# Optimization experiments

Measured on AMD Instinct MI355X. Metric: run time of the kernel, lower is better.

The kernel has to match this reference:

```python
import jax, jax.numpy as jnp
import numpy as np

D_MODEL = 1024
N_HEADS = 16
D_H = D_MODEL // N_HEADS
B, S = 2, 2048


def setup_inputs() -> dict:
    key = jax.random.key(0)
    ks = jax.random.split(key, 12)
    s = 1.0 / np.sqrt(D_MODEL)
    inp = {
        "Q": jax.random.normal(ks[0], (B, S, D_MODEL), jnp.float32),
        "K": jax.random.normal(ks[1], (B, S, D_MODEL), jnp.float32),
        "V": jax.random.normal(ks[2], (B, S, D_MODEL), jnp.float32),
        # causal mask: True means masked out (matches masked_fill semantics)
        "masked": jnp.broadcast_to(~jnp.tril(jnp.ones((S, S), bool)), (B, S, S)),
        "WQ_w": jax.random.uniform(ks[3], (D_MODEL, D_MODEL), jnp.float32, -s, s),
        "WQ_b": jax.random.uniform(ks[4], (D_MODEL,), jnp.float32, -s, s),
        "WK_w": jax.random.uniform(ks[5], (D_MODEL, D_MODEL), jnp.float32, -s, s),
        "WK_b": jax.random.uniform(ks[6], (D_MODEL,), jnp.float32, -s, s),
        "WV_w": jax.random.uniform(ks[7], (D_MODEL, D_MODEL), jnp.float32, -s, s),
        "WV_b": jax.random.uniform(ks[8], (D_MODEL,), jnp.float32, -s, s),
        "Wo_w": jax.random.uniform(ks[9], (D_MODEL, D_MODEL), jnp.float32, -s, s),
        "Wo_b": jax.random.uniform(ks[10], (D_MODEL,), jnp.float32, -s, s),
    }
    return inp


def reference(Q, K, V, masked, WQ_w, WQ_b, WK_w, WK_b, WV_w, WV_b, Wo_w, Wo_b):
    b = Q.shape[0]
    # torch Linear: y = x @ W^T + b
    def split_heads(x):
        return x.reshape(b, -1, N_HEADS, D_H).transpose(0, 2, 1, 3)  # [B,H,S,d_h]

    q = split_heads(Q @ WQ_w.T + WQ_b)
    k = split_heads(K @ WK_w.T + WK_b)
    v = split_heads(V @ WV_w.T + WV_b)

    scores = jnp.einsum("bhqd,bhkd->bhqk", q, k) / np.sqrt(D_H)
    scores = jnp.where(masked[:, None, :, :], jnp.float32(-1e9), scores)
    attn = jax.nn.softmax(scores, axis=-1)
    ctx = jnp.einsum("bhqk,bhkd->bhqd", attn, v)  # [B,H,S,d_h]
    ctx = ctx.transpose(0, 2, 1, 3).reshape(b, -1, N_HEADS * D_H)
    return ctx @ Wo_w.T + Wo_b
```

## Files before the change

### kernel.cpp

```cpp
#include <hip/hip_runtime.h>
#include <hip/hip_bf16.h>
#include <math.h>


typedef __bf16 bf16_t;
typedef bf16_t bf16x8 __attribute__((ext_vector_type(8)));
typedef bf16_t bf16x4 __attribute__((ext_vector_type(4)));
typedef float f32x4 __attribute__((ext_vector_type(4)));

#define MFMA16(a, b, c) __builtin_amdgcn_mfma_f32_16x16x32_bf16(a, b, c, 0, 0, 0)

constexpr int S_LEN = 2048;
constexpr int DMODEL = 1024;
constexpr int DHEAD = 64;
constexpr int MTOT = 2 * S_LEN;
constexpr size_t NQ = (size_t)MTOT * DMODEL;
constexpr size_t NW = (size_t)DMODEL * DMODEL;
constexpr float ESC = 0.18033688011112042f;

__device__ __forceinline__ void load_lds16(const void* g, void* l) {
  __builtin_amdgcn_global_load_lds((const __attribute__((address_space(1))) void*)g,
                                   (__attribute__((address_space(3))) void*)l, 16, 0, 0);
}

__global__ __launch_bounds__(256) void convert_all(
    const float* __restrict__ Q, const float* __restrict__ K, const float* __restrict__ V,
    const float* __restrict__ W0, const float* __restrict__ W1, const float* __restrict__ W2,
    const float* __restrict__ W3, bf16_t* __restrict__ dst) {
  const size_t i = ((size_t)blockIdx.x * 256 + threadIdx.x) * 4;
  const float* s;
  size_t off = i;
  if (off < NQ) { s = Q; }
  else if (off < 2 * NQ) { s = K; off -= NQ; }
  else if (off < 3 * NQ) { s = V; off -= 2 * NQ; }
  else {
    off -= 3 * NQ;
    if (off < NW) { s = W0; }
    else if (off < 2 * NW) { s = W1; off -= NW; }
    else if (off < 3 * NW) { s = W2; off -= 2 * NW; }
    else { s = W3; off -= 3 * NW; }
  }
  const float4 v4 = *(const float4*)(s + off);
  bf16x4 b;
  b[0] = (bf16_t)v4.x; b[1] = (bf16_t)v4.y; b[2] = (bf16_t)v4.z; b[3] = (bf16_t)v4.w;
  *(bf16x4*)(dst + i) = b;
}

template <int BK>
__device__ __forceinline__ void gemm_loop(const bf16_t* __restrict__ Ab,
                                          const bf16_t* __restrict__ Wb,
                                          bf16_t* As, bf16_t* Ws,
                                          f32x4 (&acc)[4][4], int wave, int lane) {
  constexpr int CH = BK / 8;
  constexpr int RPI = 64 / CH;
  constexpr int IPW = BK / 16;
  const int col = lane & 15, quad = lane >> 4;
  const int wm = (wave >> 1) * 64, wn = (wave & 1) * 64;
  const int srow = lane / CH;
  const int sch = lane % CH;

  for (int k0 = 0; k0 < 1024; k0 += BK) {
    __syncthreads();
#pragma unroll
    for (int i = 0; i < IPW; i++) {
      const int rbase = (i * 4 + wave) * RPI;
      const int g = sch ^ ((rbase + srow) & 7);
      load_lds16(Ab + (size_t)(rbase + srow) * 1024 + k0 + g * 8, As + rbase * BK);
      load_lds16(Wb + (size_t)(rbase + srow) * 1024 + k0 + g * 8, Ws + rbase * BK);
    }
    __syncthreads();
#pragma unroll
    for (int kc = 0; kc < BK / 32; kc++) {
      const int slot = (kc * 4 + quad) ^ (col & 7);
      bf16x8 af[4], wf[4];
#pragma unroll
      for (int i = 0; i < 4; i++) af[i] = *(const bf16x8*)&As[(wm + i * 16 + col) * BK + slot * 8];
#pragma unroll
      for (int j = 0; j < 4; j++) wf[j] = *(const bf16x8*)&Ws[(wn + j * 16 + col) * BK + slot * 8];
#pragma unroll
      for (int i = 0; i < 4; i++)
#pragma unroll
        for (int j = 0; j < 4; j++) acc[i][j] = MFMA16(af[i], wf[j], acc[i][j]);
    }
  }
}

__global__ __launch_bounds__(256, 3) void gemm_qkv(const bf16_t* __restrict__ Abase,
                                                   const bf16_t* __restrict__ Wbase,
                                                   const float* __restrict__ b0,
                                                   const float* __restrict__ b1,
                                                   const float* __restrict__ b2,
                                                   bf16_t* __restrict__ obase) {
  __shared__ bf16_t As[128 * 64];
  __shared__ bf16_t Ws[128 * 64];
  const int z = blockIdx.z;
  const int bm = blockIdx.x * 128, bn = blockIdx.y * 128;
  const int lane = threadIdx.x & 63, wave = threadIdx.x >> 6;
  const int col = lane & 15, quad = lane >> 4;
  const int wm = (wave >> 1) * 64, wn = (wave & 1) * 64;

  f32x4 acc[4][4];
#pragma unroll
  for (int i = 0; i < 4; i++)
#pragma unroll
    for (int j = 0; j < 4; j++)
#pragma unroll
      for (int r = 0; r < 4; r++) acc[i][j][r] = 0.f;

  const bf16_t* A = Abase + z * NQ + (size_t)bm * 1024;
  const bf16_t* W = Wbase + z * NW + (size_t)bn * 1024;
  const float* bias = (z == 0) ? b0 : ((z == 1) ? b1 : b2);
  bf16_t* out = obase + z * NQ;

  gemm_loop<64>(A, W, As, Ws, acc, wave, lane);

  const float esc = (z == 0) ? ESC : 1.0f;
#pragma unroll
  for (int i = 0; i < 4; i++) {
#pragma unroll
    for (int j = 0; j < 4; j++) {
      const int n = bn + wn + j * 16 + col;
      const float bv = bias[n];
      const int h = n >> 6, dh = n & 63;
      if (z < 2) {
#pragma unroll
        for (int r = 0; r < 4; r++) {
          const int m = bm + wm + i * 16 + quad * 4 + r;
          const int b = m >> 11, s = m & 2047;
          out[((size_t)((b * 16 + h) * S_LEN + s) << 6) | dh] =
              (bf16_t)((acc[i][j][r] + bv) * esc);
        }
      } else {
        const int m0 = bm + wm + i * 16 + quad * 4;
        const int b = m0 >> 11, s0 = m0 & 2047;
        bf16x4 p4;
#pragma unroll
        for (int r = 0; r < 4; r++) p4[r] = (bf16_t)(acc[i][j][r] + bv);
        *(bf16x4*)&out[(((size_t)((b * 16 + h) * DHEAD + dh)) << 11) | s0] = p4;
      }
    }
  }
}

__global__ __launch_bounds__(256, 2) void gemm_out(const bf16_t* __restrict__ A,
                                                   const bf16_t* __restrict__ W,
                                                   const float* __restrict__ bias,
                                                   float* __restrict__ out) {
  __shared__ bf16_t As[64 * 64];
  __shared__ bf16_t Ws[128 * 64];
  const int bm = blockIdx.x * 64, bn = blockIdx.y * 128;
  const int lane = threadIdx.x & 63, wave = threadIdx.x >> 6;
  const int col = lane & 15, quad = lane >> 4;
  const int wm = (wave >> 1) * 32, wn = (wave & 1) * 64;

  f32x4 acc[2][4];
#pragma unroll
  for (int i = 0; i < 2; i++)
#pragma unroll
    for (int j = 0; j < 4; j++)
#pragma unroll
      for (int r = 0; r < 4; r++) acc[i][j][r] = 0.f;

  const int srow = lane >> 3, s7 = lane & 7;
  const bf16_t* Ab = A + (size_t)bm * 1024;
  const bf16_t* Wb = W + (size_t)bn * 1024;

  for (int k0 = 0; k0 < 1024; k0 += 64) {
    __syncthreads();
#pragma unroll
    for (int i = 0; i < 2; i++) {
      const int rbase = (i * 4 + wave) * 8;
      const int g = s7 ^ srow;
      load_lds16(Ab + (size_t)(rbase + srow) * 1024 + k0 + g * 8, As + rbase * 64);
    }
#pragma unroll
    for (int i = 0; i < 4; i++) {
      const int rbase = (i * 4 + wave) * 8;
      const int g = s7 ^ srow;
      load_lds16(Wb + (size_t)(rbase + srow) * 1024 + k0 + g * 8, Ws + rbase * 64);
    }
    __syncthreads();
#pragma unroll
    for (int kc = 0; kc < 2; kc++) {
      const int slot = (kc * 4 + quad) ^ (col & 7);
      bf16x8 af[2], wf[4];
#pragma unroll
      for (int i = 0; i < 2; i++) af[i] = *(const bf16x8*)&As[(wm + i * 16 + col) * 64 + slot * 8];
#pragma unroll
      for (int j = 0; j < 4; j++) wf[j] = *(const bf16x8*)&Ws[(wn + j * 16 + col) * 64 + slot * 8];
#pragma unroll
      for (int i = 0; i < 2; i++)
#pragma unroll
        for (int j = 0; j < 4; j++) acc[i][j] = MFMA16(af[i], wf[j], acc[i][j]);
    }
  }

#pragma unroll
  for (int i = 0; i < 2; i++)
#pragma unroll
    for (int j = 0; j < 4; j++) {
      const int n = bn + wn + j * 16 + col;
      const float bv = bias[n];
#pragma unroll
      for (int r = 0; r < 4; r++) {
        const int m = bm + wm + i * 16 + quad * 4 + r;
        out[(size_t)m * DMODEL + n] = acc[i][j][r] + bv;
      }
    }
}

__global__ __launch_bounds__(256, 2) void attn(const bf16_t* __restrict__ q,
                                               const bf16_t* __restrict__ k,
                                               const bf16_t* __restrict__ vT,
                                               bf16_t* __restrict__ ctx) {
  const int bh = blockIdx.x;
  const int p = blockIdx.y;
  const int half = blockIdx.z;
  const int tA = p, tB = 15 - p;
  const int lane = threadIdx.x & 63, wave = threadIdx.x >> 6;
  const int col = lane & 15, quad = lane >> 4;

  __shared__ bf16_t Ks[2][128 * 64];
  __shared__ bf16_t Vs[2][64 * 128];
  __shared__ bf16_t Ps[4][16 * 128];

  const bf16_t* kbh = k + (size_t)bh * S_LEN * DHEAD;
  const bf16_t* vbh = vT + (size_t)bh * DHEAD * S_LEN;

  const int k_srow = lane >> 3, k_g = (lane & 7) ^ k_srow;
  const int v_row = lane >> 4, v_sl = lane & 15;
  const int qrow = half * 64 + wave * 16 + col;

  auto stage = [&](int c, int b) {
#pragma unroll
    for (int i = 0; i < 4; i++) {
      const int rbase = (wave * 4 + i) * 8;
      load_lds16(kbh + (size_t)(c * 128 + rbase + k_srow) * DHEAD + k_g * 8,
                 &Ks[b][rbase * 64]);
    }
#pragma unroll
    for (int i = 0; i < 4; i++) {
      const int dbase = (wave * 4 + i) * 4;
      const int d = dbase + v_row;
      const int g = v_sl ^ (d & 7);
      load_lds16(vbh + (size_t)d * S_LEN + c * 128 + g * 8, &Vs[b][dbase * 128]);
    }
  };

  bf16x8 aq[2];
  f32x4 o[4];
  float lsum = 0.f;
  int buf = 0;

  stage(0, 0);

  for (int it = 0; it <= 16; ++it) {
    const bool onA = (it <= tA);
    const int T = onA ? tA : tB;
    const int c = onA ? it : it - tA - 1;

    if (c == 0) {
      const bf16_t* qb = q + ((size_t)bh * S_LEN + T * 128 + qrow) * DHEAD;
      aq[0] = *(const bf16x8*)(qb + quad * 8);
      aq[1] = *(const bf16x8*)(qb + 32 + quad * 8);
      lsum = 0.f;
#pragma unroll
      for (int db = 0; db < 4; db++)
#pragma unroll
        for (int r = 0; r < 4; r++) o[db][r] = 0.f;
    }

    __syncthreads();

    if (it < 16) stage((it + 1 <= tA) ? it + 1 : it - tA, buf ^ 1);

    f32x4 sacc[8];
#pragma unroll
    for (int nb = 0; nb < 8; nb++)
#pragma unroll
      for (int r = 0; r < 4; r++) sacc[nb][r] = 0.f;
#pragma unroll
    for (int kc = 0; kc < 2; kc++) {
      const int sl = (kc * 4 + quad) ^ (col & 7);
#pragma unroll
      for (int nb = 0; nb < 8; nb++) {
        const bf16x8 bk = *(const bf16x8*)&Ks[buf][(nb * 16 + col) * 64 + sl * 8];
        sacc[nb] = MFMA16(bk, aq[kc], sacc[nb]);
      }
    }

    const bool diag = (c == T);
#pragma unroll
    for (int nb = 0; nb < 8; nb++) {
      bf16x4 p4;
#pragma unroll
      for (int r = 0; r < 4; r++) {
        float pv = exp2f(sacc[nb][r]);
        if (diag && (nb * 16 + quad * 4 + r) > qrow) pv = 0.f;
        lsum += pv;
        p4[r] = (bf16_t)pv;
      }
      const int sl = (2 * nb + (quad >> 1)) ^ (col & 7);
      *(bf16x4*)&Ps[wave][col * 128 + sl * 8 + (quad & 1) * 4] = p4;
    }

#pragma unroll
    for (int kc = 0; kc < 4; kc++) {
      const int sl = (4 * kc + quad) ^ (col & 7);
      const bf16x8 pa = *(const bf16x8*)&Ps[wave][col * 128 + sl * 8];
#pragma unroll
      for (int db = 0; db < 4; db++) {
        const bf16x8 bv = *(const bf16x8*)&Vs[buf][(db * 16 + col) * 128 + sl * 8];
        o[db] = MFMA16(bv, pa, o[db]);
      }
    }

    if (c == T) {
      float l = lsum;
      l += __shfl_xor(l, 16);
      l += __shfl_xor(l, 32);
      const float inv = 1.f / l;
      const int b = bh >> 4, h = bh & 15;
      const int qg = T * 128 + qrow;
      bf16_t* cb = ctx + ((size_t)(b * S_LEN + qg)) * DMODEL + h * DHEAD;
#pragma unroll
      for (int db = 0; db < 4; db++) {
        bf16x4 o4;
#pragma unroll
        for (int r = 0; r < 4; r++) o4[r] = (bf16_t)(o[db][r] * inv);
        *(bf16x4*)&cb[db * 16 + quad * 4] = o4;
      }
    }
    buf ^= 1;
  }
}

extern "C" void kernel_launch(void* const* d_in, const int* in_sizes, int n_in,
                              void* d_out, int out_size, void* d_ws, size_t ws_size,
                              hipStream_t stream) {
  const float* Q = (const float*)d_in[0];
  const float* K = (const float*)d_in[1];
  const float* V = (const float*)d_in[2];
  const float* WQw = (const float*)d_in[4];
  const float* WQb = (const float*)d_in[5];
  const float* WKw = (const float*)d_in[6];
  const float* WKb = (const float*)d_in[7];
  const float* WVw = (const float*)d_in[8];
  const float* WVb = (const float*)d_in[9];
  const float* Wow = (const float*)d_in[10];
  const float* Wob = (const float*)d_in[11];

  bf16_t* base = (bf16_t*)d_ws;
  bf16_t* Wc = base + 3 * NQ;
  bf16_t* qp = base + 3 * NQ + 4 * NW;
  bf16_t* ctx = base;

  const size_t total = 3 * NQ + 4 * NW;
  convert_all<<<dim3((unsigned)(total / 4 / 256)), dim3(256), 0, stream>>>(
      Q, K, V, WQw, WKw, WVw, Wow, base);

  gemm_qkv<<<dim3(32, 8, 3), dim3(256), 0, stream>>>(base, Wc, WQb, WKb, WVb, qp);
  attn<<<dim3(32, 8, 2), dim3(256), 0, stream>>>(qp, qp + NQ, qp + 2 * NQ, ctx);
  gemm_out<<<dim3(64, 8), dim3(256), 0, stream>>>(ctx, Wc + 3 * NW, Wob, (float*)d_out);
}
```

Measured before the change: 232.0 us.

## Rework attention to 64-row tiles with direct global loads; double-buffer output GEMM

The attention kernel drops the paired-tile LDS staging of K and V and instead has each block handle one 64-query tile. K and V fragments are read straight from global memory into MFMA operands, with a grid of 32x32 blocks and higher occupancy. The output projection GEMM moves to 128x128 tiles with double-buffered LDS staging, and the QKV GEMM loop is specialised to BK=64. Removing LDS staging in attention trades shared-memory traffic and barriers for uncoalesced global/L2 reads, which may cost more than the extra parallelism gains.

```diff
diff --git a/kernel.cpp b/kernel.cpp
--- a/kernel.cpp
+++ b/kernel.cpp
@@ -46,37 +46,33 @@
   *(bf16x4*)(dst + i) = b;
 }
 
-template <int BK>
-__device__ __forceinline__ void gemm_loop(const bf16_t* __restrict__ Ab,
-                                          const bf16_t* __restrict__ Wb,
-                                          bf16_t* As, bf16_t* Ws,
-                                          f32x4 (&acc)[4][4], int wave, int lane) {
-  constexpr int CH = BK / 8;
-  constexpr int RPI = 64 / CH;
-  constexpr int IPW = BK / 16;
+__device__ __forceinline__ void gemm_loop64(const bf16_t* __restrict__ Ab,
+                                            const bf16_t* __restrict__ Wb,
+                                            bf16_t* As, bf16_t* Ws,
+                                            f32x4 (&acc)[4][4], int wave, int lane) {
   const int col = lane & 15, quad = lane >> 4;
   const int wm = (wave >> 1) * 64, wn = (wave & 1) * 64;
-  const int srow = lane / CH;
-  const int sch = lane % CH;
-
-  for (int k0 = 0; k0 < 1024; k0 += BK) {
+  const int srow = lane >> 3;
+  const int s7 = lane & 7;
+
+  for (int k0 = 0; k0 < 1024; k0 += 64) {
     __syncthreads();
 #pragma unroll
-    for (int i = 0; i < IPW; i++) {
-      const int rbase = (i * 4 + wave) * RPI;
-      const int g = sch ^ ((rbase + srow) & 7);
-      load_lds16(Ab + (size_t)(rbase + srow) * 1024 + k0 + g * 8, As + rbase * BK);
-      load_lds16(Wb + (size_t)(rbase + srow) * 1024 + k0 + g * 8, Ws + rbase * BK);
+    for (int i = 0; i < 4; i++) {
+      const int rbase = (i * 4 + wave) * 8;
+      const int g = s7 ^ ((rbase + srow) & 7);
+      load_lds16(Ab + (size_t)(rbase + srow) * 1024 + k0 + g * 8, As + rbase * 64);
+      load_lds16(Wb + (size_t)(rbase + srow) * 1024 + k0 + g * 8, Ws + rbase * 64);
     }
     __syncthreads();
 #pragma unroll
-    for (int kc = 0; kc < BK / 32; kc++) {
+    for (int kc = 0; kc < 2; kc++) {
       const int slot = (kc * 4 + quad) ^ (col & 7);
       bf16x8 af[4], wf[4];
 #pragma unroll
-      for (int i = 0; i < 4; i++) af[i] = *(const bf16x8*)&As[(wm + i * 16 + col) * BK + slot * 8];
-#pragma unroll
-      for (int j = 0; j < 4; j++) wf[j] = *(const bf16x8*)&Ws[(wn + j * 16 + col) * BK + slot * 8];
+      for (int i = 0; i < 4; i++) af[i] = *(const bf16x8*)&As[(wm + i * 16 + col) * 64 + slot * 8];
+#pragma unroll
+      for (int j = 0; j < 4; j++) wf[j] = *(const bf16x8*)&Ws[(wn + j * 16 + col) * 64 + slot * 8];
 #pragma unroll
       for (int i = 0; i < 4; i++)
 #pragma unroll
@@ -112,7 +108,7 @@
   const float* bias = (z == 0) ? b0 : ((z == 1) ? b1 : b2);
   bf16_t* out = obase + z * NQ;
 
-  gemm_loop<64>(A, W, As, Ws, acc, wave, lane);
+  gemm_loop64(A, W, As, Ws, acc, wave, lane);
 
   const float esc = (z == 0) ? ESC : 1.0f;
 #pragma unroll
@@ -142,61 +138,65 @@
   }
 }
 
-__global__ __launch_bounds__(256, 2) void gemm_out(const bf16_t* __restrict__ A,
-                                                   const bf16_t* __restrict__ W,
-                                                   const float* __restrict__ bias,
-                                                   float* __restrict__ out) {
-  __shared__ bf16_t As[64 * 64];
-  __shared__ bf16_t Ws[128 * 64];
-  const int bm = blockIdx.x * 64, bn = blockIdx.y * 128;
+__global__ __launch_bounds__(256) void gemm_out(const bf16_t* __restrict__ A,
+                                                const bf16_t* __restrict__ W,
+                                                const float* __restrict__ bias,
+                                                float* __restrict__ out) {
+  __shared__ bf16_t As[2][128 * 64];
+  __shared__ bf16_t Ws[2][128 * 64];
+  const int bm = blockIdx.x * 128, bn = blockIdx.y * 128;
   const int lane = threadIdx.x & 63, wave = threadIdx.x >> 6;
   const int col = lane & 15, quad = lane >> 4;
-  const int wm = (wave >> 1) * 32, wn = (wave & 1) * 64;
-
-  f32x4 acc[2][4];
-#pragma unroll
-  for (int i = 0; i < 2; i++)
-#pragma unroll
-    for (int j = 0; j < 4; j++)
-#pragma unroll
-      for (int r = 0; r < 4; r++) acc[i][j][r] = 0.f;
-
+  const int wm = (wave >> 1) * 64, wn = (wave & 1) * 64;
   const int srow = lane >> 3, s7 = lane & 7;
+
   const bf16_t* Ab = A + (size_t)bm * 1024;
   const bf16_t* Wb = W + (size_t)bn * 1024;
 
-  for (int k0 = 0; k0 < 1024; k0 += 64) {
-    __syncthreads();
-#pragma unroll
-    for (int i = 0; i < 2; i++) {
-      const int rbase = (i * 4 + wave) * 8;
-      const int g = s7 ^ srow;
-      load_lds16(Ab + (size_t)(rbase + srow) * 1024 + k0 + g * 8, As + rbase * 64);
-    }
+  auto stage = [&](int k0, int b) {
 #pragma unroll
     for (int i = 0; i < 4; i++) {
       const int rbase = (i * 4 + wave) * 8;
-      const int g = s7 ^ srow;
-      load_lds16(Wb + (size_t)(rbase + srow) * 1024 + k0 + g * 8, Ws + rbase * 64);
-    }
+      const int g = s7 ^ ((rbase + srow) & 7);
+      load_lds16(Ab + (size_t)(rbase + srow) * 1024 + k0 + g * 8, &As[b][rbase * 64]);
+      load_lds16(Wb + (size_t)(rbase + srow) * 1024 + k0 + g * 8, &Ws[b][rbase * 64]);
+    }
+  };
+
+  f32x4 acc[4][4];
+#pragma unroll
+  for (int i = 0; i < 4; i++)
+#pragma unroll
+    for (int j = 0; j < 4; j++)
+#pragma unroll
+      for (int r = 0; r < 4; r++) acc[i][j][r] = 0.f;
+
+  stage(0, 0);
+  int buf = 0;
+  for (int it = 0; it < 16; ++it) {
     __syncthreads();
+    if (it < 15) stage((it + 1) * 64, buf ^ 1);
 #pragma unroll
     for (int kc = 0; kc < 2; kc++) {
       const int slot = (kc * 4 + quad) ^ (col & 7);
-      bf16x8 af[2], wf[4];
-#pragma unroll
-      for (int i = 0; i < 2; i++) af[i] = *(const bf16x8*)&As[(wm + i * 16 + col) * 64 + slot * 8];
-#pragma unroll
-      for (int j = 0; j < 4; j++) wf[j] = *(const bf16x8*)&Ws[(wn + j * 16 + col) * 64 + slot * 8];
-#pragma unroll
-      for (int i = 0; i < 2; i++)
+      bf16x8 af[4], wf[4];
+#pragma unroll
+      for (int i = 0; i < 4; i++)
+        af[i] = *(const bf16x8*)&As[buf][(wm + i * 16 + col) * 64 + slot * 8];
+#pragma unroll
+      for (int j = 0; j < 4; j++)
+        wf[j] = *(const bf16x8*)&Ws[buf][(wn + j * 16 + col) * 64 + slot * 8];
+#pragma unroll
+      for (int i = 0; i < 4; i++)
 #pragma unroll
         for (int j = 0; j < 4; j++) acc[i][j] = MFMA16(af[i], wf[j], acc[i][j]);
     }
-  }
-
-#pragma unroll
-  for (int i = 0; i < 2; i++)
+    __syncthreads();
+    buf ^= 1;
+  }
+
+#pragma unroll
+  for (int i = 0; i < 4; i++)
 #pragma unroll
     for (int j = 0; j < 4; j++) {
       const int n = bn + wn + j * 16 + col;
@@ -209,129 +209,97 @@
     }
 }
 
-__global__ __launch_bounds__(256, 2) void attn(const bf16_t* __restrict__ q,
+__global__ __launch_bounds__(256, 4) void attn(const bf16_t* __restrict__ q,
                                                const bf16_t* __restrict__ k,
                                                const bf16_t* __restrict__ vT,
                                                bf16_t* __restrict__ ctx) {
   const int bh = blockIdx.x;
-  const int p = blockIdx.y;
-  const int half = blockIdx.z;
-  const int tA = p, tB = 15 - p;
+  const int T = 31 - blockIdx.y;
   const int lane = threadIdx.x & 63, wave = threadIdx.x >> 6;
   const int col = lane & 15, quad = lane >> 4;
 
-  __shared__ bf16_t Ks[2][128 * 64];
-  __shared__ bf16_t Vs[2][64 * 128];
-  __shared__ bf16_t Ps[4][16 * 128];
+  __shared__ bf16_t Ps[4][16 * 64];
 
   const bf16_t* kbh = k + (size_t)bh * S_LEN * DHEAD;
   const bf16_t* vbh = vT + (size_t)bh * DHEAD * S_LEN;
 
-  const int k_srow = lane >> 3, k_g = (lane & 7) ^ k_srow;
-  const int v_row = lane >> 4, v_sl = lane & 15;
-  const int qrow = half * 64 + wave * 16 + col;
-
-  auto stage = [&](int c, int b) {
-#pragma unroll
-    for (int i = 0; i < 4; i++) {
-      const int rbase = (wave * 4 + i) * 8;
-      load_lds16(kbh + (size_t)(c * 128 + rbase + k_srow) * DHEAD + k_g * 8,
-                 &Ks[b][rbase * 64]);
-    }
-#pragma unroll
-    for (int i = 0; i < 4; i++) {
-      const int dbase = (wave * 4 + i) * 4;
-      const int d = dbase + v_row;
-      const int g = v_sl ^ (d & 7);
-      load_lds16(vbh + (size_t)d * S_LEN + c * 128 + g * 8, &Vs[b][dbase * 128]);
-    }
-  };
-
-  bf16x8 aq[2];
+  const int ql = wave * 16 + col;
+  const int qg = T * 64 + ql;
+  const bf16_t* qb = q + ((size_t)bh * S_LEN + qg) * DHEAD;
+  const bf16x8 aq0 = *(const bf16x8*)(qb + quad * 8);
+  const bf16x8 aq1 = *(const bf16x8*)(qb + 32 + quad * 8);
+
   f32x4 o[4];
+#pragma unroll
+  for (int db = 0; db < 4; db++)
+#pragma unroll
+    for (int r = 0; r < 4; r++) o[db][r] = 0.f;
   float lsum = 0.f;
-  int buf = 0;
-
-  stage(0, 0);
-
-  for (int it = 0; it <= 16; ++it) {
-    const bool onA = (it <= tA);
-    const int T = onA ? tA : tB;
-    const int c = onA ? it : it - tA - 1;
-
-    if (c == 0) {
-      const bf16_t* qb = q + ((size_t)bh * S_LEN + T * 128 + qrow) * DHEAD;
-      aq[0] = *(const bf16x8*)(qb + quad * 8);
-      aq[1] = *(const bf16x8*)(qb + 32 + quad * 8);
-      lsum = 0.f;
-#pragma unroll
-      for (int db = 0; db < 4; db++)
-#pragma unroll
-        for (int r = 0; r < 4; r++) o[db][r] = 0.f;
-    }
-
-    __syncthreads();
-
-    if (it < 16) stage((it + 1 <= tA) ? it + 1 : it - tA, buf ^ 1);
-
-    f32x4 sacc[8];
-#pragma unroll
-    for (int nb = 0; nb < 8; nb++)
+
+  for (int c = 0; c <= T; ++c) {
+    const bf16_t* kc0 = kbh + (size_t)c * 64 * DHEAD;
+
+    f32x4 sacc[4];
+#pragma unroll
+    for (int nb = 0; nb < 4; nb++)
 #pragma unroll
       for (int r = 0; r < 4; r++) sacc[nb][r] = 0.f;
 #pragma unroll
     for (int kc = 0; kc < 2; kc++) {
-      const int sl = (kc * 4 + quad) ^ (col & 7);
-#pragma unroll
-      for (int nb = 0; nb < 8; nb++) {
-        const bf16x8 bk = *(const bf16x8*)&Ks[buf][(nb * 16 + col) * 64 + sl * 8];
-        sacc[nb] = MFMA16(bk, aq[kc], sacc[nb]);
-      }
-    }
-
-    const bool diag = (c == T);
-#pragma unroll
-    for (int nb = 0; nb < 8; nb++) {
+      const bf16x8 aqc = kc ? aq1 : aq0;
+#pragma unroll
+      for (int nb = 0; nb < 4; nb++) {
+        const bf16x8 ak =
+            *(const bf16x8*)(kc0 + (size_t)(nb * 16 + col) * DHEAD + kc * 32 + quad * 8);
+        sacc[nb] = MFMA16(ak, aqc, sacc[nb]);
+      }
+    }
+
+#pragma unroll
+    for (int nb = 0; nb < 4; nb++) {
+      f32x4 pv;
+#pragma unroll
+      for (int r = 0; r < 4; r++) pv[r] = __builtin_amdgcn_exp2f(sacc[nb][r]);
+      if (c == T) {
+#pragma unroll
+        for (int r = 0; r < 4; r++)
+          if (nb * 16 + quad * 4 + r > ql) pv[r] = 0.f;
+      }
       bf16x4 p4;
 #pragma unroll
       for (int r = 0; r < 4; r++) {
-        float pv = exp2f(sacc[nb][r]);
-        if (diag && (nb * 16 + quad * 4 + r) > qrow) pv = 0.f;
-        lsum += pv;
-        p4[r] = (bf16_t)pv;
+        lsum += pv[r];
+        p4[r] = (bf16_t)pv[r];
       }
       const int sl = (2 * nb + (quad >> 1)) ^ (col & 7);
-      *(bf16x4*)&Ps[wave][col * 128 + sl * 8 + (quad & 1) * 4] = p4;
-    }
-
-#pragma unroll
-    for (int kc = 0; kc < 4; kc++) {
+      *(bf16x4*)&Ps[wave][col * 64 + sl * 8 + (quad & 1) * 4] = p4;
+    }
+
+#pragma unroll
+    for (int kc = 0; kc < 2; kc++) {
       const int sl = (4 * kc + quad) ^ (col & 7);
-      const bf16x8 pa = *(const bf16x8*)&Ps[wave][col * 128 + sl * 8];
+      const bf16x8 pa = *(const bf16x8*)&Ps[wave][col * 64 + sl * 8];
 #pragma unroll
       for (int db = 0; db < 4; db++) {
-        const bf16x8 bv = *(const bf16x8*)&Vs[buf][(db * 16 + col) * 128 + sl * 8];
-        o[db] = MFMA16(bv, pa, o[db]);
-      }
-    }
-
-    if (c == T) {
-      float l = lsum;
-      l += __shfl_xor(l, 16);
-      l += __shfl_xor(l, 32);
-      const float inv = 1.f / l;
-      const int b = bh >> 4, h = bh & 15;
-      const int qg = T * 128 + qrow;
-      bf16_t* cb = ctx + ((size_t)(b * S_LEN + qg)) * DMODEL + h * DHEAD;
-#pragma unroll
-      for (int db = 0; db < 4; db++) {
-        bf16x4 o4;
-#pragma unroll
-        for (int r = 0; r < 4; r++) o4[r] = (bf16_t)(o[db][r] * inv);
-        *(bf16x4*)&cb[db * 16 + quad * 4] = o4;
-      }
-    }
-    buf ^= 1;
+        const bf16x8 av = *(const bf16x8*)(vbh + (size_t)(db * 16 + col) * S_LEN +
+                                           c * 64 + kc * 32 + quad * 8);
+        o[db] = MFMA16(av, pa, o[db]);
+      }
+    }
+  }
+
+  float l = lsum;
+  l += __shfl_xor(l, 16);
+  l += __shfl_xor(l, 32);
+  const float inv = 1.f / l;
+  const int b = bh >> 4, h = bh & 15;
+  bf16_t* cb = ctx + ((size_t)(b * S_LEN + qg)) * DMODEL + h * DHEAD;
+#pragma unroll
+  for (int db = 0; db < 4; db++) {
+    bf16x4 o4;
+#pragma unroll
+    for (int r = 0; r < 4; r++) o4[r] = (bf16_t)(o[db][r] * inv);
+    *(bf16x4*)&cb[db * 16 + quad * 4] = o4;
   }
 }
 
@@ -360,6 +328,6 @@
       Q, K, V, WQw, WKw, WVw, Wow, base);
 
   gemm_qkv<<<dim3(32, 8, 3), dim3(256), 0, stream>>>(base, Wc, WQb, WKb, WVb, qp);
-  attn<<<dim3(32, 8, 2), dim3(256), 0, stream>>>(qp, qp + NQ, qp + 2 * NQ, ctx);
-  gemm_out<<<dim3(64, 8), dim3(256), 0, stream>>>(ctx, Wc + 3 * NW, Wob, (float*)d_out);
-}
+  attn<<<dim3(32, 32), dim3(256), 0, stream>>>(qp, qp + NQ, qp + 2 * NQ, ctx);
+  gemm_out<<<dim3(32, 8), dim3(256), 0, stream>>>(ctx, Wc + 3 * NW, Wob, (float*)d_out);
+}
```

Result: slower. 332.5 us (+43.4%).
